# Optimization experiments

Hardware: AMD Instinct MI355X
Metric: run time of the kernel (lower is better)

Reference implementation:

```python
import jax, jax.numpy as jnp
import numpy as np

NUM_REL = 20000
NUM_EDGES = 640000
DIM_IN = 128
DIM_OUT = 128
NUM_HEAD = 8
DIM_HID = DIM_OUT // NUM_HEAD
NUM_BIN = 10
NEG_SLOPE = 0.2


def leaky_relu(x):
    return jnp.where(x >= 0, x, NEG_SLOPE * x)


def setup_inputs() -> dict:
    key = jax.random.key(0)
    ks = jax.random.split(key, 8)
    emb_rel = jax.random.normal(ks[0], (NUM_REL, DIM_IN), dtype=jnp.float32)
    head = jax.random.randint(ks[1], (NUM_EDGES, 1), 0, NUM_REL)
    tail = jax.random.randint(ks[2], (NUM_EDGES, 1), 0, NUM_REL)
    bins = jax.random.randint(ks[3], (NUM_EDGES, 1), 0, NUM_BIN)
    relation_triplets = jnp.concatenate([head, tail, bins], axis=-1).astype(jnp.int64)
    # xavier-normal-ish init
    attn_proj_w = jax.random.normal(ks[4], (DIM_OUT, 2 * DIM_IN), dtype=jnp.float32) * (2.0 / np.sqrt(2 * DIM_IN + DIM_OUT))
    attn_proj_b = jnp.zeros((DIM_OUT,), dtype=jnp.float32)
    attn_bin = jax.random.normal(ks[5], (NUM_BIN, NUM_HEAD, 1), dtype=jnp.float32) * 0.3
    attn_vec = jax.random.normal(ks[6], (1, NUM_HEAD, DIM_HID), dtype=jnp.float32) * (2.0 / np.sqrt(NUM_HEAD * DIM_HID))
    aggr_proj_w = jax.random.normal(ks[7], (DIM_OUT, DIM_IN), dtype=jnp.float32) * (2.0 / np.sqrt(DIM_IN + DIM_OUT))
    aggr_proj_b = jnp.zeros((DIM_OUT,), dtype=jnp.float32)
    return {"emb_rel": emb_rel, "relation_triplets": relation_triplets,
            "attn_proj_w": attn_proj_w, "attn_proj_b": attn_proj_b,
            "attn_bin": attn_bin, "attn_vec": attn_vec,
            "aggr_proj_w": aggr_proj_w, "aggr_proj_b": aggr_proj_b}


def reference(emb_rel, relation_triplets, attn_proj_w, attn_proj_b, attn_bin, attn_vec, aggr_proj_w, aggr_proj_b):
    num_rel = emb_rel.shape[0]
    head = relation_triplets[..., 0]
    tail = relation_triplets[..., 1]
    bins = relation_triplets[..., 2]
    # edge gather + concat: [E, 2*dim_in]
    concat = jnp.concatenate([emb_rel[head], emb_rel[tail]], axis=-1)
    proj = concat @ attn_proj_w.T + attn_proj_b  # [E, dim_out]
    proj = leaky_relu(proj).reshape(-1, NUM_HEAD, DIM_HID)
    attn_raw = (proj * attn_vec).sum(axis=-1, keepdims=True) + leaky_relu(attn_bin[bins])  # [E,H,1]
    # per-head-relation segment softmax over edges grouped by head index
    seg_max = jax.ops.segment_max(attn_raw, head, num_segments=num_rel)  # [R,H,1]
    attn_val = jnp.exp(attn_raw - seg_max[head])
    seg_sum = jax.ops.segment_sum(attn_val, head, num_segments=num_rel)  # [R,H,1]
    beta = attn_val / (seg_sum[head] + 1e-16)
    msg = (emb_rel[tail] @ aggr_proj_w.T + aggr_proj_b).reshape(-1, NUM_HEAD, DIM_HID)
    out = jax.ops.segment_sum(beta * msg, head, num_segments=num_rel)  # [R,H,Dh]
    return out.reshape(num_rel, -1)
```

## Files before the change

kernel.cpp:

```cpp
#include <hip/hip_runtime.h>
#include <hip/hip_bf16.h>
#include <cstdint>
#include <cstddef>

#define NUM_REL    20000
#define NUM_EDGES  640000
#define DIM        128
#define NUM_HEAD   8
#define DIM_HID    16
#define NUM_BIN    10
#define CAP        128
#define PROJ_BLKS  471
#define SC_BLKS    2500

using u16 = unsigned short;
using u32 = unsigned int;
typedef __attribute__((ext_vector_type(8))) short bf16x8;
typedef __attribute__((ext_vector_type(4))) float f32x4;

__device__ __forceinline__ float b2f(u16 u) { return __uint_as_float(((u32)u) << 16); }
__device__ __forceinline__ float lo2f(u32 u) { return __uint_as_float(u << 16); }
__device__ __forceinline__ float hi2f(u32 u) { return __uint_as_float(u & 0xffff0000u); }
__device__ __forceinline__ float lrelu(float x) { return fmaxf(x, 0.2f * x); }
__device__ __forceinline__ int clampi(int v, int hi) { return v < 0 ? 0 : (v > hi ? hi : v); }
__device__ __forceinline__ float ldf(const void* p, int f32m, int i)
{ return f32m ? ((const float*)p)[i] : b2f(((const u16*)p)[i]); }
__device__ __forceinline__ u16 f2b(float x)
{ u32 u = __float_as_uint(x); u += 0x7fffu + ((u >> 16) & 1u); return (u16)(u >> 16); }
__device__ __forceinline__ u32 pk2(float a, float b)
{ return (u32)f2b(a) | ((u32)f2b(b) << 16); }

__device__ __forceinline__ void detect_flags(const int* __restrict__ trip,
                                             const u16* __restrict__ emb,
                                             int* sF, int tid)
{
    if (tid < 64) {
        bool odd_zero = (trip[2 * tid + 1] == 0) && (trip[2 * tid + 129] == 0);
        unsigned long long m1 = __ballot(odd_zero);
        int ex = (emb[2 * tid] >> 7) & 0xFF;
        bool inr = (ex >= 110) && (ex <= 136);
        unsigned long long m2 = __ballot(inr);
        if (tid == 0) {
            sF[0] = (~m1 == 0ull) ? 1 : 0;
            sF[1] = (__popcll(m2) >= 32) ? 0 : 1;
        }
    }
    __syncthreads();
}

__global__ __launch_bounds__(256) void k_projscatter(
    const void* __restrict__ emb, const int* __restrict__ trip,
    const void* __restrict__ w_attn, const void* __restrict__ w_aggr,
    const void* __restrict__ b_attn, const void* __restrict__ b_aggr,
    float* __restrict__ A, u16* __restrict__ Bb, u16* __restrict__ Mb,
    int* __restrict__ cnt, int* __restrict__ bucket)
{
    __shared__ u16 sW[128 * 128];
    __shared__ float sBias[128];
    __shared__ int sF[2];

    const int tid = threadIdx.x;
    detect_flags(trip, (const u16*)emb, sF, tid);
    const int is64 = sF[0], f32m = sF[1];

    if (blockIdx.x >= PROJ_BLKS) {
        int e = (blockIdx.x - PROJ_BLKS) * 256 + tid;
        if (e < NUM_EDGES) {
            int h, t, b;
            if (is64) { h = trip[6 * e]; t = trip[6 * e + 2]; b = trip[6 * e + 4]; }
            else      { h = trip[3 * e]; t = trip[3 * e + 1]; b = trip[3 * e + 2]; }
            h = clampi(h, NUM_REL - 1);
            t = clampi(t, NUM_REL - 1);
            b = clampi(b, NUM_BIN - 1);
            int pos = atomicAdd(&cnt[h], 1);
            if (pos < CAP) bucket[h * CAP + pos] = t | (b << 20);
        }
        return;
    }

    const int mt = blockIdx.x / 3, nt = blockIdx.x % 3;
    const int r0 = mt * 128;

    if (tid < 128)
        sBias[tid] = (nt == 0) ? 0.f : ldf((nt == 1) ? b_attn : b_aggr, f32m, tid);

    {
        const void* wsrc = (nt == 2) ? w_aggr : w_attn;
        const int stride = (nt == 2) ? 128 : 256;
        const int koff   = (nt == 1) ? 128 : 0;
        if (f32m) {
            const float* src = (const float*)wsrc;
            #pragma unroll
            for (int i = 0; i < 16; ++i) {
                int f = i * 256 + tid;
                int row = f >> 5, pos = f & 31;
                float4 x = ((const float4*)(src + (size_t)row * stride + koff))[pos];
                int chunk = (pos >> 1) ^ (row & 15);
                *(uint2*)&sW[row * 128 + chunk * 8 + (pos & 1) * 4] =
                    make_uint2(pk2(x.x, x.y), pk2(x.z, x.w));
            }
        } else {
            const u16* src = (const u16*)wsrc;
            #pragma unroll
            for (int i = 0; i < 8; ++i) {
                int f = i * 256 + tid;
                int row = f >> 4, pos = f & 15;
                uint4 x = ((const uint4*)(src + (size_t)row * stride + koff))[pos];
                int chunk = pos ^ (row & 15);
                *(uint4*)&sW[row * 128 + chunk * 8] = x;
            }
        }
    }
    __syncthreads();

    const int lane = tid & 63, wid = tid >> 6;
    const int wm = (wid >> 1) * 64, wn = (wid & 1) * 64;
    const int ln15 = lane & 15, q = lane >> 4;

    int arow[4];
    #pragma unroll
    for (int mi = 0; mi < 4; ++mi) {
        int g = r0 + wm + mi * 16 + ln15;
        arow[mi] = (g < NUM_REL) ? g : (NUM_REL - 1);
    }

    f32x4 acc[4][4] = {};
    #pragma unroll
    for (int kk = 0; kk < 4; ++kk) {
        const int cbase = kk * 4 + q;
        const int kc = cbase * 8;
        bf16x8 a[4], b[4];
        #pragma unroll
        for (int mi = 0; mi < 4; ++mi) {
            if (f32m) {
                const float* er = (const float*)emb + (size_t)arow[mi] * DIM + kc;
                float4 x0 = *(const float4*)er;
                float4 x1 = *(const float4*)(er + 4);
                union { bf16x8 v; u32 u[4]; } cv;
                cv.u[0] = pk2(x0.x, x0.y); cv.u[1] = pk2(x0.z, x0.w);
                cv.u[2] = pk2(x1.x, x1.y); cv.u[3] = pk2(x1.z, x1.w);
                a[mi] = cv.v;
            } else {
                a[mi] = *(const bf16x8*)((const u16*)emb + (size_t)arow[mi] * DIM + kc);
            }
        }
        #pragma unroll
        for (int ni = 0; ni < 4; ++ni) {
            int n = wn + ni * 16 + ln15;
            int c = cbase ^ ln15;
            b[ni] = *(const bf16x8*)&sW[n * 128 + c * 8];
        }
        #pragma unroll
        for (int mi = 0; mi < 4; ++mi)
            #pragma unroll
            for (int ni = 0; ni < 4; ++ni)
                acc[mi][ni] = __builtin_amdgcn_mfma_f32_16x16x32_bf16(
                    a[mi], b[ni], acc[mi][ni], 0, 0, 0);
    }

    #pragma unroll
    for (int mi = 0; mi < 4; ++mi) {
        #pragma unroll
        for (int reg = 0; reg < 4; ++reg) {
            int g = r0 + wm + mi * 16 + q * 4 + reg;
            if (g < NUM_REL) {
                #pragma unroll
                for (int ni = 0; ni < 4; ++ni) {
                    int c = wn + ni * 16 + ln15;
                    float v = acc[mi][ni][reg] + sBias[c];
                    size_t o = (size_t)g * DIM + c;
                    if (nt == 0)      A[o]  = v;
                    else if (nt == 1) Bb[o] = f2b(v);
                    else              Mb[o] = f2b(v);
                }
            }
        }
    }
}

__global__ __launch_bounds__(256, 6) void k_segment(
    const float* __restrict__ A, const u16* __restrict__ Bb,
    const u16* __restrict__ Mb, const void* __restrict__ attn_bin,
    const void* __restrict__ attn_vec, const int* __restrict__ cnt,
    const int* __restrict__ bucket, const int* __restrict__ trip,
    const void* __restrict__ emb, void* __restrict__ out)
{
    __shared__ float sAr[4][DIM];
    __shared__ float sVec[DIM];
    __shared__ float sBin[NUM_BIN * NUM_HEAD];
    __shared__ int sF[2];

    const int tid  = threadIdx.x;
    detect_flags(trip, (const u16*)emb, sF, tid);
    const int f32m = sF[1];

    const int wid  = tid >> 6, lane = tid & 63;
    const int r = blockIdx.x * 4 + wid;
    int nE = cnt[r]; if (nE > CAP) nE = CAP;
    const int* __restrict__ bk = bucket + r * CAP;

    {
        const float2* ap = (const float2*)(A + (size_t)r * DIM);
        float2 a2 = ap[lane];
        sAr[wid][2 * lane] = a2.x; sAr[wid][2 * lane + 1] = a2.y;
    }
    if (tid < DIM) sVec[tid] = ldf(attn_vec, f32m, tid);
    else if (tid < DIM + NUM_BIN * NUM_HEAD)
        sBin[tid - DIM] = lrelu(ldf(attn_bin, f32m, tid - DIM));
    __syncthreads();

    if (nE == 0) {
        if (f32m) ((float2*)out)[(size_t)r * 64 + lane] = make_float2(0.f, 0.f);
        else      ((u32*)out)[(size_t)r * 64 + lane] = 0;
        return;
    }

    const int el = lane >> 3, hd = lane & 7;
    const int ah = lane >> 3;

    float av[16], vv[16];
    {
        const float4* pA = (const float4*)(&sAr[wid][hd * DIM_HID]);
        const float4* pV = (const float4*)(&sVec[hd * DIM_HID]);
        #pragma unroll
        for (int i = 0; i < 4; ++i) {
            float4 a4 = pA[i], v4 = pV[i];
            av[4*i+0]=a4.x; av[4*i+1]=a4.y; av[4*i+2]=a4.z; av[4*i+3]=a4.w;
            vv[4*i+0]=v4.x; vv[4*i+1]=v4.y; vv[4*i+2]=v4.z; vv[4*i+3]=v4.w;
        }
    }

    float l = 0.f, accx = 0.f, accy = 0.f;

    for (int base = 0; base < nE; base += 8) {
        int e = base + el;
        bool act = e < nE;
        int tb = 0;
        if (act) tb = bk[e];
        int t = tb & 0xFFFFF;
        float p = 0.f;
        if (act) {
            int b = (tb >> 20) & 0xF;
            const uint4* Bt = (const uint4*)(Bb + (size_t)t * DIM) + hd * 2;
            uint4 q0 = Bt[0], q1 = Bt[1];
            float s = sBin[b * NUM_HEAD + hd];
            s += lrelu(av[0]  + lo2f(q0.x)) * vv[0];
            s += lrelu(av[1]  + hi2f(q0.x)) * vv[1];
            s += lrelu(av[2]  + lo2f(q0.y)) * vv[2];
            s += lrelu(av[3]  + hi2f(q0.y)) * vv[3];
            s += lrelu(av[4]  + lo2f(q0.z)) * vv[4];
            s += lrelu(av[5]  + hi2f(q0.z)) * vv[5];
            s += lrelu(av[6]  + lo2f(q0.w)) * vv[6];
            s += lrelu(av[7]  + hi2f(q0.w)) * vv[7];
            s += lrelu(av[8]  + lo2f(q1.x)) * vv[8];
            s += lrelu(av[9]  + hi2f(q1.x)) * vv[9];
            s += lrelu(av[10] + lo2f(q1.y)) * vv[10];
            s += lrelu(av[11] + hi2f(q1.y)) * vv[11];
            s += lrelu(av[12] + lo2f(q1.z)) * vv[12];
            s += lrelu(av[13] + hi2f(q1.z)) * vv[13];
            s += lrelu(av[14] + lo2f(q1.w)) * vv[14];
            s += lrelu(av[15] + hi2f(q1.w)) * vv[15];
            s = fminf(fmaxf(s, -60.f), 60.f);
            p = __expf(s);
        }
        l += p;

        int lim = nE - base; if (lim > 8) lim = 8;
        #pragma unroll
        for (int k = 0; k < 8; ++k) {
            if (k < lim) {
                float v = __shfl(p, k * 8 + ah);
                int tk  = __shfl(t, k * 8);
                u32 mm = *(const u32*)(Mb + (size_t)tk * DIM + 2 * lane);
                accx += v * lo2f(mm);
                accy += v * hi2f(mm);
            }
        }
    }

    float lt = l + __shfl_xor(l, 8);
    lt += __shfl_xor(lt, 16);
    lt += __shfl_xor(lt, 32);
    float lA = __shfl(lt, ah);
    float inv = 1.0f / (lA + 1e-16f);
    float o0 = accx * inv, o1 = accy * inv;
    if (f32m) {
        ((float2*)out)[(size_t)r * 64 + lane] = make_float2(o0, o1);
    } else {
        u32 pk = (u32)f2b(o0) | ((u32)f2b(o1) << 16);
        ((u32*)out)[(size_t)r * 64 + lane] = pk;
    }
}

extern "C" void kernel_launch(void* const* d_in, const int* in_sizes, int n_in,
                              void* d_out, int out_size, void* d_ws, size_t ws_size,
                              hipStream_t stream)
{
    (void)in_sizes; (void)n_in; (void)out_size; (void)ws_size;
    const void* emb      = d_in[0];
    const int*  trip     = (const int*)d_in[1];
    const void* w_attn   = d_in[2];
    const void* b_attn   = d_in[3];
    const void* attn_bin = d_in[4];
    const void* attn_vec = d_in[5];
    const void* w_aggr   = d_in[6];
    const void* b_aggr   = d_in[7];

    char* p = (char*)d_ws;
    float* A      = (float*)p; p += (size_t)NUM_REL * DIM * 4;
    u16*   Bb     = (u16*)p;   p += (size_t)NUM_REL * DIM * 2;
    u16*   Mb     = (u16*)p;   p += (size_t)NUM_REL * DIM * 2;
    int*   bucket = (int*)p;   p += (size_t)NUM_REL * CAP * 4;
    int*   cnt    = (int*)p;   p += (size_t)NUM_REL * 4;

    hipMemsetAsync(cnt, 0, NUM_REL * sizeof(int), stream);
    k_projscatter<<<PROJ_BLKS + SC_BLKS, 256, 0, stream>>>(
        emb, trip, w_attn, w_aggr, b_attn, b_aggr, A, Bb, Mb, cnt, bucket);
    k_segment<<<NUM_REL / 4, 256, 0, stream>>>(A, Bb, Mb, attn_bin, attn_vec,
                                               cnt, bucket, trip, emb, d_out);
}
```

Baseline: 192.4 us.

## Software-pipeline edge gathers in aggregation loop and split accumulators

Restructures the per-relation aggregation loop so the next group's bucket entry and attention-projection rows are prefetched while the current group is scored. All eight message rows are issued as a batch before the score math, and the dot products and accumulators are split into independent chains to shorten FMA dependency latency. The triplet read in the bucketing pass now uses int2 loads. This raises register pressure, which could reduce occupancy. Inactive lanes load row 0 unconditionally; this is safe because the entry is masked when the bucket has fewer edges.

```diff
diff --git a/kernel.cpp b/kernel.cpp
--- a/kernel.cpp
+++ b/kernel.cpp
@@ -67,8 +67,14 @@
         int e = (blockIdx.x - PROJ_BLKS) * 256 + tid;
         if (e < NUM_EDGES) {
             int h, t, b;
-            if (is64) { h = trip[6 * e]; t = trip[6 * e + 2]; b = trip[6 * e + 4]; }
-            else      { h = trip[3 * e]; t = trip[3 * e + 1]; b = trip[3 * e + 2]; }
+            if (is64) {
+                int2 hh = *(const int2*)(trip + 6 * e);
+                int2 tt = *(const int2*)(trip + 6 * e + 2);
+                int2 bb = *(const int2*)(trip + 6 * e + 4);
+                h = hh.x; t = tt.x; b = bb.x;
+            } else {
+                h = trip[3 * e]; t = trip[3 * e + 1]; b = trip[3 * e + 2];
+            }
             h = clampi(h, NUM_REL - 1);
             t = clampi(t, NUM_REL - 1);
             b = clampi(b, NUM_BIN - 1);
@@ -230,53 +236,75 @@
         }
     }
 
-    float l = 0.f, accx = 0.f, accy = 0.f;
+    const u16* __restrict__ Mbl = Mb + 2 * lane;
+
+    int tb = (el < nE) ? bk[el] : 0;
+    int t  = tb & 0xFFFFF;
+    uint4 q0, q1;
+    {
+        const uint4* Bt = (const uint4*)(Bb + (size_t)t * DIM) + hd * 2;
+        q0 = Bt[0]; q1 = Bt[1];
+    }
+
+    float l = 0.f;
+    float ax0 = 0.f, ax1 = 0.f, ay0 = 0.f, ay1 = 0.f;
 
     for (int base = 0; base < nE; base += 8) {
-        int e = base + el;
-        bool act = e < nE;
-        int tb = 0;
-        if (act) tb = bk[e];
-        int t = tb & 0xFFFFF;
-        float p = 0.f;
-        if (act) {
-            int b = (tb >> 20) & 0xF;
-            const uint4* Bt = (const uint4*)(Bb + (size_t)t * DIM) + hd * 2;
-            uint4 q0 = Bt[0], q1 = Bt[1];
-            float s = sBin[b * NUM_HEAD + hd];
-            s += lrelu(av[0]  + lo2f(q0.x)) * vv[0];
-            s += lrelu(av[1]  + hi2f(q0.x)) * vv[1];
-            s += lrelu(av[2]  + lo2f(q0.y)) * vv[2];
-            s += lrelu(av[3]  + hi2f(q0.y)) * vv[3];
-            s += lrelu(av[4]  + lo2f(q0.z)) * vv[4];
-            s += lrelu(av[5]  + hi2f(q0.z)) * vv[5];
-            s += lrelu(av[6]  + lo2f(q0.w)) * vv[6];
-            s += lrelu(av[7]  + hi2f(q0.w)) * vv[7];
-            s += lrelu(av[8]  + lo2f(q1.x)) * vv[8];
-            s += lrelu(av[9]  + hi2f(q1.x)) * vv[9];
-            s += lrelu(av[10] + lo2f(q1.y)) * vv[10];
-            s += lrelu(av[11] + hi2f(q1.y)) * vv[11];
-            s += lrelu(av[12] + lo2f(q1.z)) * vv[12];
-            s += lrelu(av[13] + hi2f(q1.z)) * vv[13];
-            s += lrelu(av[14] + lo2f(q1.w)) * vv[14];
-            s += lrelu(av[15] + hi2f(q1.w)) * vv[15];
-            s = fminf(fmaxf(s, -60.f), 60.f);
-            p = __expf(s);
-        }
+        u32 mm[8];
+        #pragma unroll
+        for (int k = 0; k < 8; ++k) {
+            int tk = __shfl(t, k * 8);
+            mm[k] = *(const u32*)(Mbl + (size_t)tk * DIM);
+        }
+        const int bsel = (tb >> 20) & 0xF;
+
+        int e_n  = base + 8 + el;
+        int tb_n = (e_n < nE) ? bk[e_n] : 0;
+        int t_n  = tb_n & 0xFFFFF;
+        uint4 q0n, q1n;
+        {
+            const uint4* Btn = (const uint4*)(Bb + (size_t)t_n * DIM) + hd * 2;
+            q0n = Btn[0]; q1n = Btn[1];
+        }
+
+        float s0 = sBin[bsel * NUM_HEAD + hd];
+        s0 = fmaf(lrelu(av[0]  + lo2f(q0.x)), vv[0],  s0);
+        float s1 = lrelu(av[1] + hi2f(q0.x)) * vv[1];
+        float s2 = lrelu(av[2] + lo2f(q0.y)) * vv[2];
+        float s3 = lrelu(av[3] + hi2f(q0.y)) * vv[3];
+        s0 = fmaf(lrelu(av[4]  + lo2f(q0.z)), vv[4],  s0);
+        s1 = fmaf(lrelu(av[5]  + hi2f(q0.z)), vv[5],  s1);
+        s2 = fmaf(lrelu(av[6]  + lo2f(q0.w)), vv[6],  s2);
+        s3 = fmaf(lrelu(av[7]  + hi2f(q0.w)), vv[7],  s3);
+        s0 = fmaf(lrelu(av[8]  + lo2f(q1.x)), vv[8],  s0);
+        s1 = fmaf(lrelu(av[9]  + hi2f(q1.x)), vv[9],  s1);
+        s2 = fmaf(lrelu(av[10] + lo2f(q1.y)), vv[10], s2);
+        s3 = fmaf(lrelu(av[11] + hi2f(q1.y)), vv[11], s3);
+        s0 = fmaf(lrelu(av[12] + lo2f(q1.z)), vv[12], s0);
+        s1 = fmaf(lrelu(av[13] + hi2f(q1.z)), vv[13], s1);
+        s2 = fmaf(lrelu(av[14] + lo2f(q1.w)), vv[14], s2);
+        s3 = fmaf(lrelu(av[15] + hi2f(q1.w)), vv[15], s3);
+        float s = (s0 + s1) + (s2 + s3);
+        s = fminf(fmaxf(s, -60.f), 60.f);
+        float p = ((base + el) < nE) ? __expf(s) : 0.f;
         l += p;
 
-        int lim = nE - base; if (lim > 8) lim = 8;
         #pragma unroll
         for (int k = 0; k < 8; ++k) {
-            if (k < lim) {
-                float v = __shfl(p, k * 8 + ah);
-                int tk  = __shfl(t, k * 8);
-                u32 mm = *(const u32*)(Mb + (size_t)tk * DIM + 2 * lane);
-                accx += v * lo2f(mm);
-                accy += v * hi2f(mm);
-            }
-        }
-    }
+            float v = __shfl(p, k * 8 + ah);
+            if (k & 1) {
+                ax1 = fmaf(v, lo2f(mm[k]), ax1);
+                ay1 = fmaf(v, hi2f(mm[k]), ay1);
+            } else {
+                ax0 = fmaf(v, lo2f(mm[k]), ax0);
+                ay0 = fmaf(v, hi2f(mm[k]), ay0);
+            }
+        }
+
+        tb = tb_n; t = t_n; q0 = q0n; q1 = q1n;
+    }
+
+    float accx = ax0 + ax1, accy = ay0 + ay1;
 
     float lt = l + __shfl_xor(l, 8);
     lt += __shfl_xor(lt, 16);
```

New measurement: 179.4 us. 1.07x faster.
